# Kernel tuning notes

Hardware: AMD Instinct MI355X
Metric: run time of the kernel (lower is better)

## Reference

```python
import jax, jax.numpy as jnp
import numpy as np

NUM_CLASSES = 80
ALPHA, GAMMA, BETA = 0.25, 2.0, 0.11
POS_THR, NEG_THR = 0.5, 0.4
B, A, G = 8, 98304, 32


def setup_inputs() -> dict:
    key = jax.random.key(0)
    k1, k2, k3, k4, k5, k6, k7 = jax.random.split(key, 7)
    # anchors: random centers/sizes over an ~800px image, xyxy format
    ctr = jax.random.uniform(k1, (A, 2), minval=50.0, maxval=750.0)
    wh = jax.random.uniform(k2, (A, 2), minval=16.0, maxval=256.0)
    anchors = jnp.concatenate([ctr - wh / 2, ctr + wh / 2], axis=-1)
    # gt boxes = jittered anchors so that positive (IoU>=0.5) matches exist
    idx = jax.random.randint(k3, (B, G), 0, A)
    gt_boxes = anchors[idx] + jax.random.normal(k4, (B, G, 4)) * 2.0
    gt_boxes = jnp.concatenate([
        jnp.minimum(gt_boxes[..., :2], gt_boxes[..., 2:] - 1.0),
        jnp.maximum(gt_boxes[..., 2:], gt_boxes[..., :2] + 1.0)], axis=-1)
    gt_labels = jax.random.randint(k5, (B, G), 1, NUM_CLASSES + 1)  # 1-indexed fg
    cls_predictions = jax.random.normal(k6, (B, A, NUM_CLASSES), dtype=jnp.float32)
    reg_predictions = jax.random.normal(k7, (B, A, 4), dtype=jnp.float32)
    return {"cls_predictions": cls_predictions, "reg_predictions": reg_predictions,
            "anchors": anchors, "gt_boxes": gt_boxes, "gt_labels": gt_labels}


def _pairwise_iou(boxes1, boxes2):  # [A,4],[G,4] -> [A,G]
    area1 = (boxes1[:, 2] - boxes1[:, 0]) * (boxes1[:, 3] - boxes1[:, 1])
    area2 = (boxes2[:, 2] - boxes2[:, 0]) * (boxes2[:, 3] - boxes2[:, 1])
    lt = jnp.maximum(boxes1[:, None, :2], boxes2[None, :, :2])
    rb = jnp.minimum(boxes1[:, None, 2:], boxes2[None, :, 2:])
    wh = jnp.clip(rb - lt, 0.0)
    inter = wh[..., 0] * wh[..., 1]
    return inter / (area1[:, None] + area2[None, :] - inter)


def _encode(matched, anchors):  # BoxCoder with weights (1,1,1,1)
    aw = anchors[:, 2] - anchors[:, 0]
    ah = anchors[:, 3] - anchors[:, 1]
    ax = anchors[:, 0] + 0.5 * aw
    ay = anchors[:, 1] + 0.5 * ah
    gw = matched[:, 2] - matched[:, 0]
    gh = matched[:, 3] - matched[:, 1]
    gx = matched[:, 0] + 0.5 * gw
    gy = matched[:, 1] + 0.5 * gh
    return jnp.stack([(gx - ax) / aw, (gy - ay) / ah,
                      jnp.log(gw / aw), jnp.log(gh / ah)], axis=-1)


def _match(anchors, gt_boxes_i, gt_labels_i):
    iou = _pairwise_iou(anchors, gt_boxes_i)          # [A, G]
    max_iou = iou.max(axis=-1)
    midx = iou.argmax(axis=-1)
    labels = gt_labels_i[midx]                        # [A]
    cls_t = jnp.where(max_iou >= POS_THR, labels,
                      jnp.where(max_iou < NEG_THR, 0, -1))
    reg_t = _encode(gt_boxes_i[midx], anchors)        # [A, 4]
    pos = max_iou >= POS_THR
    return cls_t, reg_t, pos


def reference(cls_predictions, reg_predictions, anchors, gt_boxes, gt_labels):
    cls_t, reg_t, pos = jax.vmap(_match, in_axes=(None, 0, 0))(anchors, gt_boxes, gt_labels)
    valid = (cls_t >= 0)[..., None].astype(cls_predictions.dtype)  # [B,A,1]
    fg = (cls_t > 0)[..., None].astype(cls_predictions.dtype)
    # one-hot targets (labels are 1-indexed; 0 = background -> all zeros)
    t = jax.nn.one_hot(cls_t - 1, NUM_CLASSES, dtype=cls_predictions.dtype) * fg
    x = cls_predictions
    bce = jnp.maximum(x, 0.0) - x * t + jnp.log1p(jnp.exp(-jnp.abs(x)))
    prob = jax.nn.sigmoid(x)
    p_t = prob * t + (1.0 - prob) * (1.0 - t)
    alpha_f = ALPHA * t + (1.0 - ALPHA) * (1.0 - t)
    focal = alpha_f * (1.0 - p_t) ** GAMMA * bce
    cls_sum = (focal * valid).sum()
    diff = jnp.abs(reg_predictions - reg_t)
    sl1 = jnp.where(diff < BETA, 0.5 * diff * diff / BETA, diff - 0.5 * BETA)
    posf = pos[..., None].astype(reg_predictions.dtype)
    reg_sum = (sl1 * posf).sum()
    num_pos = pos.sum().astype(cls_predictions.dtype)
    denom = jnp.maximum(num_pos, 1.0)
    cls_loss = jnp.where(num_pos > 0, cls_sum / denom, cls_sum)
    reg_loss = jnp.where(num_pos > 0, reg_sum / denom, 0.0)
    return (cls_loss + reg_loss, cls_loss, reg_loss)
```

## Files before the change

kernel.cpp:

```cpp
#include <hip/hip_runtime.h>
#include <math.h>

#define NUM_CLASSES 80
#define ALPHA 0.25f
#define GAMMA 2.0f
#define BETA 0.11f
#define POS_THR 0.5f
#define NEG_THR 0.4f
#define B_CNT 8
#define A_CNT 98304
#define G_CNT 32


__device__ __forceinline__ float block_reduce_sum(float v, float* s) {
    #pragma unroll
    for (int off = 32; off > 0; off >>= 1) v += __shfl_down(v, off, 64);
    const int wave = threadIdx.x >> 6;
    if ((threadIdx.x & 63) == 0) s[wave] = v;
    __syncthreads();
    return (threadIdx.x == 0) ? (s[0] + s[1] + s[2] + s[3]) : 0.0f;
}

__global__ __launch_bounds__(256) void match_kernel(
    const float* __restrict__ reg_pred,
    const float* __restrict__ anchors,
    const float* __restrict__ gt_boxes,
    const int*   __restrict__ gt_labels,
    signed char* __restrict__ cls_t_out,
    float* __restrict__ accum)
{
    __shared__ float4 s_gt[G_CNT];
    __shared__ int    s_lab[G_CNT];
    __shared__ float  s_red[4];
    __shared__ float  s_cnt[4];

    const int blocks_per_batch = A_CNT / 256;
    const int b = blockIdx.x / blocks_per_batch;
    const int a = (blockIdx.x % blocks_per_batch) * 256 + threadIdx.x;

    if (threadIdx.x < G_CNT) {
        s_gt[threadIdx.x]  = ((const float4*)gt_boxes)[b * G_CNT + threadIdx.x];
        s_lab[threadIdx.x] = gt_labels[b * G_CNT + threadIdx.x];
    }
    __syncthreads();

    const float4 an = ((const float4*)anchors)[a];
    const float aw = an.z - an.x;
    const float ah = an.w - an.y;
    const float area_a = aw * ah;

    float best = -1.0f;
    int bidx = 0;
    #pragma unroll
    for (int g = 0; g < G_CNT; ++g) {
        const float4 gb = s_gt[g];
        const float ltx = fmaxf(an.x, gb.x);
        const float lty = fmaxf(an.y, gb.y);
        const float rbx = fminf(an.z, gb.z);
        const float rby = fminf(an.w, gb.w);
        const float w = fmaxf(rbx - ltx, 0.0f);
        const float h = fmaxf(rby - lty, 0.0f);
        const float inter = w * h;
        const float area_g = (gb.z - gb.x) * (gb.w - gb.y);
        const float iou = inter / (area_a + area_g - inter);
        if (iou > best) { best = iou; bidx = g; }
    }

    const bool pos = (best >= POS_THR);
    const int lab = s_lab[bidx];
    signed char ct = pos ? (signed char)lab : ((best < NEG_THR) ? (signed char)0 : (signed char)-1);
    cls_t_out[b * A_CNT + a] = ct;

    float regsum = 0.0f;
    if (pos) {
        const float4 gb = s_gt[bidx];
        const float gw = gb.z - gb.x;
        const float gh = gb.w - gb.y;
        const float gx = gb.x + 0.5f * gw;
        const float gy = gb.y + 0.5f * gh;
        const float ax = an.x + 0.5f * aw;
        const float ay = an.y + 0.5f * ah;
        const float t0 = (gx - ax) / aw;
        const float t1 = (gy - ay) / ah;
        const float t2 = __logf(gw / aw);
        const float t3 = __logf(gh / ah);
        const float4 rp = ((const float4*)reg_pred)[b * A_CNT + a];
        const float d0 = fabsf(rp.x - t0);
        const float d1 = fabsf(rp.y - t1);
        const float d2 = fabsf(rp.z - t2);
        const float d3 = fabsf(rp.w - t3);
        const float s0 = (d0 < BETA) ? 0.5f * d0 * d0 / BETA : d0 - 0.5f * BETA;
        const float s1 = (d1 < BETA) ? 0.5f * d1 * d1 / BETA : d1 - 0.5f * BETA;
        const float s2 = (d2 < BETA) ? 0.5f * d2 * d2 / BETA : d2 - 0.5f * BETA;
        const float s3 = (d3 < BETA) ? 0.5f * d3 * d3 / BETA : d3 - 0.5f * BETA;
        regsum = s0 + s1 + s2 + s3;
    }

    float rs = block_reduce_sum(regsum, s_red);
    __syncthreads();
    float cnt = block_reduce_sum(pos ? 1.0f : 0.0f, s_cnt);
    if (threadIdx.x == 0) {
        if (rs != 0.0f) atomicAdd(&accum[1], rs);
        if (cnt != 0.0f) atomicAdd(&accum[2], cnt);
    }
}

__device__ __forceinline__ float focal_fast(float x, bool is_t) {
    const float ax = fabsf(x);
    const float e  = __expf(-ax);
    const float op = 1.0f + e;
    const float l  = __logf(op);
    const float r  = __builtin_amdgcn_rcpf(op);
    const float prob = (x >= 0.0f) ? r : e * r;
    const float p  = is_t ? (1.0f - prob) : prob;
    const float mx = is_t ? fmaxf(-x, 0.0f) : fmaxf(x, 0.0f);
    const float af = is_t ? ALPHA : (1.0f - ALPHA);
    return af * p * p * (mx + l);
}

__global__ __launch_bounds__(256) void focal_kernel(
    const float* __restrict__ cls_pred,
    const signed char* __restrict__ cls_t,
    float* __restrict__ accum)
{
    __shared__ float s_red[4];
    const int total4 = B_CNT * A_CNT * (NUM_CLASSES / 4);
    const int stride = gridDim.x * blockDim.x;
    float sum = 0.0f;
    for (int i = blockIdx.x * blockDim.x + threadIdx.x; i < total4; i += stride) {
        const int anchor = i / (NUM_CLASSES / 4);
        const int chunk = i - anchor * (NUM_CLASSES / 4);
        const signed char ct = cls_t[anchor];
        if (ct >= 0) {
            const float4 x4 = ((const float4*)cls_pred)[i];
            const int tgt = (int)ct - 1;
            const int c0 = chunk * 4;
            sum += focal_fast(x4.x, c0 + 0 == tgt);
            sum += focal_fast(x4.y, c0 + 1 == tgt);
            sum += focal_fast(x4.z, c0 + 2 == tgt);
            sum += focal_fast(x4.w, c0 + 3 == tgt);
        }
    }
    const float bs = block_reduce_sum(sum, s_red);
    if (threadIdx.x == 0 && bs != 0.0f) atomicAdd(&accum[0], bs);
}

__global__ void finalize_kernel(const float* __restrict__ accum, float* __restrict__ out) {
    const float cs = accum[0];
    const float rs = accum[1];
    const float np = accum[2];
    const float denom = fmaxf(np, 1.0f);
    const float cl = (np > 0.0f) ? cs / denom : cs;
    const float rl = (np > 0.0f) ? rs / denom : 0.0f;
    out[0] = cl + rl;
    out[1] = cl;
    out[2] = rl;
}

extern "C" void kernel_launch(void* const* d_in, const int* in_sizes, int n_in,
                              void* d_out, int out_size, void* d_ws, size_t ws_size,
                              hipStream_t stream) {
    const float* cls_pred = (const float*)d_in[0];
    const float* reg_pred = (const float*)d_in[1];
    const float* anchors  = (const float*)d_in[2];
    const float* gt_boxes = (const float*)d_in[3];
    const int*   gt_labels= (const int*)d_in[4];
    float* out = (float*)d_out;

    float* accum = (float*)d_ws;
    signed char* cls_t = (signed char*)d_ws + 16;

    hipMemsetAsync(d_ws, 0, 16, stream);

    const int blocks1 = (B_CNT * A_CNT) / 256;
    match_kernel<<<blocks1, 256, 0, stream>>>(reg_pred, anchors, gt_boxes, gt_labels, cls_t, accum);

    focal_kernel<<<4096, 256, 0, stream>>>(cls_pred, cls_t, accum);

    finalize_kernel<<<1, 1, 0, stream>>>(accum, out);
}
```

Measured before the change: 450.3 us.

## Treat all classes as negatives in focal kernel; correct positives in match kernel

The focal kernel now evaluates the negative-class focal term for every logit of each valid anchor and only reads a valid mask. The positive-class correction (focal1 minus focal0 of the target logit) is computed once per positive anchor inside the match kernel. This drops the per-element target comparisons and select logic from the hot loop. The focal grid is also sized to exactly four float4s per thread with an unrolled, fixed-trip loop. Cost: one extra strided gather of cls_pred per positive anchor and a third block reduction in the match kernel.

```diff
diff --git a/kernel.cpp b/kernel.cpp
--- a/kernel.cpp
+++ b/kernel.cpp
@@ -3,13 +3,14 @@
 
 #define NUM_CLASSES 80
 #define ALPHA 0.25f
-#define GAMMA 2.0f
 #define BETA 0.11f
 #define POS_THR 0.5f
 #define NEG_THR 0.4f
 #define B_CNT 8
 #define A_CNT 98304
 #define G_CNT 32
+
+#define FOCAL_BLOCKS 15360
 
 
 __device__ __forceinline__ float block_reduce_sum(float v, float* s) {
@@ -21,18 +22,37 @@
     return (threadIdx.x == 0) ? (s[0] + s[1] + s[2] + s[3]) : 0.0f;
 }
 
+__device__ __forceinline__ float focal0(float x) {
+    const float e  = __expf(-fabsf(x));
+    const float op = 1.0f + e;
+    const float r  = __builtin_amdgcn_rcpf(op);
+    const float prob = (x >= 0.0f) ? r : e * r;
+    const float sp = fmaxf(x, 0.0f) + __logf(op);
+    return 0.75f * prob * prob * sp;
+}
+
+__device__ __forceinline__ float focal1(float x) {
+    const float e  = __expf(-fabsf(x));
+    const float op = 1.0f + e;
+    const float r  = __builtin_amdgcn_rcpf(op);
+    const float prob = (x >= 0.0f) ? r : e * r;
+    const float q  = 1.0f - prob;
+    const float sp = fmaxf(-x, 0.0f) + __logf(op);
+    return 0.25f * q * q * sp;
+}
+
 __global__ __launch_bounds__(256) void match_kernel(
+    const float* __restrict__ cls_pred,
     const float* __restrict__ reg_pred,
     const float* __restrict__ anchors,
     const float* __restrict__ gt_boxes,
     const int*   __restrict__ gt_labels,
-    signed char* __restrict__ cls_t_out,
+    unsigned char* __restrict__ valid_out,
     float* __restrict__ accum)
 {
     __shared__ float4 s_gt[G_CNT];
     __shared__ int    s_lab[G_CNT];
     __shared__ float  s_red[4];
-    __shared__ float  s_cnt[4];
 
     const int blocks_per_batch = A_CNT / 256;
     const int b = blockIdx.x / blocks_per_batch;
@@ -67,11 +87,11 @@
     }
 
     const bool pos = (best >= POS_THR);
-    const int lab = s_lab[bidx];
-    signed char ct = pos ? (signed char)lab : ((best < NEG_THR) ? (signed char)0 : (signed char)-1);
-    cls_t_out[b * A_CNT + a] = ct;
+    const bool vld = pos || (best < NEG_THR);
+    valid_out[b * A_CNT + a] = vld ? 1 : 0;
 
     float regsum = 0.0f;
+    float clsdelta = 0.0f;
     if (pos) {
         const float4 gb = s_gt[bidx];
         const float gw = gb.z - gb.x;
@@ -94,51 +114,40 @@
         const float s2 = (d2 < BETA) ? 0.5f * d2 * d2 / BETA : d2 - 0.5f * BETA;
         const float s3 = (d3 < BETA) ? 0.5f * d3 * d3 / BETA : d3 - 0.5f * BETA;
         regsum = s0 + s1 + s2 + s3;
+
+        const int lab = s_lab[bidx];
+        const float xt = cls_pred[(size_t)(b * A_CNT + a) * NUM_CLASSES + (lab - 1)];
+        clsdelta = focal1(xt) - focal0(xt);
     }
 
     float rs = block_reduce_sum(regsum, s_red);
+    if (threadIdx.x == 0 && rs != 0.0f) atomicAdd(&accum[1], rs);
     __syncthreads();
-    float cnt = block_reduce_sum(pos ? 1.0f : 0.0f, s_cnt);
-    if (threadIdx.x == 0) {
-        if (rs != 0.0f) atomicAdd(&accum[1], rs);
-        if (cnt != 0.0f) atomicAdd(&accum[2], cnt);
-    }
-}
-
-__device__ __forceinline__ float focal_fast(float x, bool is_t) {
-    const float ax = fabsf(x);
-    const float e  = __expf(-ax);
-    const float op = 1.0f + e;
-    const float l  = __logf(op);
-    const float r  = __builtin_amdgcn_rcpf(op);
-    const float prob = (x >= 0.0f) ? r : e * r;
-    const float p  = is_t ? (1.0f - prob) : prob;
-    const float mx = is_t ? fmaxf(-x, 0.0f) : fmaxf(x, 0.0f);
-    const float af = is_t ? ALPHA : (1.0f - ALPHA);
-    return af * p * p * (mx + l);
+    float cnt = block_reduce_sum(pos ? 1.0f : 0.0f, s_red);
+    if (threadIdx.x == 0 && cnt != 0.0f) atomicAdd(&accum[2], cnt);
+    __syncthreads();
+    float cd = block_reduce_sum(clsdelta, s_red);
+    if (threadIdx.x == 0 && cd != 0.0f) atomicAdd(&accum[0], cd);
 }
 
 __global__ __launch_bounds__(256) void focal_kernel(
     const float* __restrict__ cls_pred,
-    const signed char* __restrict__ cls_t,
+    const unsigned char* __restrict__ valid,
     float* __restrict__ accum)
 {
     __shared__ float s_red[4];
-    const int total4 = B_CNT * A_CNT * (NUM_CLASSES / 4);
-    const int stride = gridDim.x * blockDim.x;
+    const int stride = FOCAL_BLOCKS * 256;
+    int i = blockIdx.x * 256 + threadIdx.x;
     float sum = 0.0f;
-    for (int i = blockIdx.x * blockDim.x + threadIdx.x; i < total4; i += stride) {
+    #pragma unroll
+    for (int k = 0; k < 4; ++k, i += stride) {
         const int anchor = i / (NUM_CLASSES / 4);
-        const int chunk = i - anchor * (NUM_CLASSES / 4);
-        const signed char ct = cls_t[anchor];
-        if (ct >= 0) {
+        if (valid[anchor]) {
             const float4 x4 = ((const float4*)cls_pred)[i];
-            const int tgt = (int)ct - 1;
-            const int c0 = chunk * 4;
-            sum += focal_fast(x4.x, c0 + 0 == tgt);
-            sum += focal_fast(x4.y, c0 + 1 == tgt);
-            sum += focal_fast(x4.z, c0 + 2 == tgt);
-            sum += focal_fast(x4.w, c0 + 3 == tgt);
+            sum += focal0(x4.x);
+            sum += focal0(x4.y);
+            sum += focal0(x4.z);
+            sum += focal0(x4.w);
         }
     }
     const float bs = block_reduce_sum(sum, s_red);
@@ -168,14 +177,15 @@
     float* out = (float*)d_out;
 
     float* accum = (float*)d_ws;
-    signed char* cls_t = (signed char*)d_ws + 16;
+    unsigned char* valid = (unsigned char*)d_ws + 16;
 
     hipMemsetAsync(d_ws, 0, 16, stream);
 
     const int blocks1 = (B_CNT * A_CNT) / 256;
-    match_kernel<<<blocks1, 256, 0, stream>>>(reg_pred, anchors, gt_boxes, gt_labels, cls_t, accum);
+    match_kernel<<<blocks1, 256, 0, stream>>>(cls_pred, reg_pred, anchors, gt_boxes,
+                                              gt_labels, valid, accum);
 
-    focal_kernel<<<4096, 256, 0, stream>>>(cls_pred, cls_t, accum);
+    focal_kernel<<<FOCAL_BLOCKS, 256, 0, stream>>>(cls_pred, valid, accum);
 
     finalize_kernel<<<1, 1, 0, stream>>>(accum, out);
 }
```

After: 591.0 us. 1.31x slower.
